# Kernel tuning notes

Measured on AMD Instinct MI355X. Metric: run time of the kernel, lower is better.

Reference implementation:

```python
import jax, jax.numpy as jnp
import numpy as np

NUM_HEADS = 16
D_MODEL = 1024
TEMPERATURE = D_MODEL ** 0.5  # note: module uses d_model**0.5, not head_dim**0.5


def setup_inputs() -> dict:
    key = jax.random.key(0)
    ks = jax.random.split(key, 8)
    B, T, D = 2, 2048, D_MODEL
    q = jax.random.normal(ks[0], (B, T, D), dtype=jnp.float32)
    k = jax.random.normal(ks[1], (B, T, D), dtype=jnp.float32)
    v = jax.random.normal(ks[2], (B, T, D), dtype=jnp.float32)
    # causal mask (tril) as suggested by the module docstring
    mask = jnp.tril(jnp.ones((T, T), dtype=bool))
    s = 1.0 / np.sqrt(D)
    Wq = jax.random.normal(ks[3], (D, D), dtype=jnp.float32) * s
    Wk = jax.random.normal(ks[4], (D, D), dtype=jnp.float32) * s
    Wv = jax.random.normal(ks[5], (D, D), dtype=jnp.float32) * s
    Wc = jax.random.normal(ks[6], (D, D), dtype=jnp.float32) * s
    return {"q": q, "k": k, "v": v, "Wq": Wq, "Wk": Wk, "Wv": Wv, "Wc": Wc, "mask": mask}


def reference(q, k, v, Wq, Wk, Wv, Wc, mask):
    B, T, D = q.shape
    H = NUM_HEADS
    hd = D // H
    # torch Linear (no bias): y = x @ W.T ; then split heads -> [B,H,T,hd]
    def proj(x, W):
        return (x @ W.T).reshape(B, T, H, hd).transpose(0, 2, 1, 3)
    qh, kh, vh = proj(q, Wq), proj(k, Wk), proj(v, Wv)
    # scores [B,H,T,T]
    scores = jnp.einsum("bhqd,bhkd->bhqk", qh / TEMPERATURE, kh)
    scores = jnp.where(mask, scores, -jnp.inf)
    attention = jax.nn.softmax(scores, axis=-1)  # dropout = identity (eval)
    out = jnp.einsum("bhqk,bhkd->bhqd", attention, vh)
    out = out.transpose(0, 2, 1, 3).reshape(B, T, D)
    out = out @ Wc.T  # combine projection; dropout = identity (eval)
    return (out, attention)
```

## Files before the change

kernel.cpp:

```cpp
#include <hip/hip_runtime.h>
#include <stdint.h>

typedef unsigned short u16;
typedef __bf16 bf16x8 __attribute__((ext_vector_type(8)));
typedef float f32x4 __attribute__((ext_vector_type(4)));

#define MFMA16(a, b, c) __builtin_amdgcn_mfma_f32_16x16x32_bf16((a), (b), (c), 0, 0, 0)

__device__ __forceinline__ u16 f2bf(float f) {
  union { __bf16 h; u16 u; } v;
  v.h = (__bf16)f;
  return v.u;
}

__device__ __forceinline__ float expf_c(float x) {
  return __expf(fmaxf(x, -80.0f));
}

struct Cvt6Args {
  const float* s0; const float* s1; const float* s2;
  const float* s3; const float* s4; const float* s5;
  u16* d0; u16* d1; u16* d2; u16* d3; u16* d4; u16* d5;
};

__global__ __launch_bounds__(256) void cvt6(Cvt6Args a) {
  const int z = blockIdx.y;
  const float* s; u16* d; int n8;
  if (z == 0)      { s = a.s0; d = a.d0; n8 = (4 * 1024 * 1024) / 8; }
  else if (z == 1) { s = a.s1; d = a.d1; n8 = (4 * 1024 * 1024) / 8; }
  else if (z == 2) { s = a.s2; d = a.d2; n8 = (4 * 1024 * 1024) / 8; }
  else if (z == 3) { s = a.s3; d = a.d3; n8 = (1024 * 1024) / 8; }
  else if (z == 4) { s = a.s4; d = a.d4; n8 = (1024 * 1024) / 8; }
  else             { s = a.s5; d = a.d5; n8 = (1024 * 1024) / 8; }
  const int i = blockIdx.x * 256 + threadIdx.x;
  if (i >= n8) return;
  float4 f0 = ((const float4*)s)[2 * i];
  float4 f1 = ((const float4*)s)[2 * i + 1];
  ushort4 h0, h1;
  h0.x = f2bf(f0.x); h0.y = f2bf(f0.y); h0.z = f2bf(f0.z); h0.w = f2bf(f0.w);
  h1.x = f2bf(f1.x); h1.y = f2bf(f1.y); h1.z = f2bf(f1.z); h1.w = f2bf(f1.w);
  ((ushort4*)d)[2 * i] = h0;
  ((ushort4*)d)[2 * i + 1] = h1;
}

__global__ __launch_bounds__(256) void cvt_one(const float* __restrict__ s,
                                               u16* __restrict__ d) {
  const int i = blockIdx.x * 256 + threadIdx.x;
  if (i >= (1024 * 1024) / 8) return;
  float4 f0 = ((const float4*)s)[2 * i];
  float4 f1 = ((const float4*)s)[2 * i + 1];
  ushort4 h0, h1;
  h0.x = f2bf(f0.x); h0.y = f2bf(f0.y); h0.z = f2bf(f0.z); h0.w = f2bf(f0.w);
  h1.x = f2bf(f1.x); h1.y = f2bf(f1.y); h1.z = f2bf(f1.z); h1.w = f2bf(f1.w);
  ((ushort4*)d)[2 * i] = h0;
  ((ushort4*)d)[2 * i + 1] = h1;
}

__device__ __forceinline__ void gemm_core(const u16* __restrict__ X,
                                          const u16* __restrict__ W,
                                          void* __restrict__ Yv, float scale,
                                          int omode) {
  __shared__ __align__(16) u16 lA[128 * 40];
  __shared__ __align__(16) u16 lB[128 * 40];
  const int tid = threadIdx.x;
  const int lane = tid & 63, w = tid >> 6;
  const int l15 = lane & 15, quad = lane >> 4;
  const int wm = (w >> 1) * 64, wn = (w & 1) * 64;
  const int m0 = blockIdx.x * 128, n0 = blockIdx.y * 128;

  f32x4 acc[4][4];
#pragma unroll
  for (int m = 0; m < 4; ++m)
#pragma unroll
    for (int n = 0; n < 4; ++n) acc[m][n] = (f32x4){0.f, 0.f, 0.f, 0.f};

  const int brow = tid >> 2, bseg = (tid & 3) * 8;

  for (int kk = 0; kk < 1024; kk += 32) {
    __syncthreads();
#pragma unroll
    for (int p = 0; p < 2; ++p) {
      int row = p * 64 + brow;
      *(uint4*)&lA[row * 40 + bseg] =
          *(const uint4*)&X[(size_t)(m0 + row) * 1024 + kk + bseg];
      *(uint4*)&lB[row * 40 + bseg] =
          *(const uint4*)&W[(size_t)(n0 + row) * 1024 + kk + bseg];
    }
    __syncthreads();
    bf16x8 af[4], bfr[4];
#pragma unroll
    for (int m = 0; m < 4; ++m)
      af[m] = *(const bf16x8*)&lA[(wm + m * 16 + l15) * 40 + quad * 8];
#pragma unroll
    for (int n = 0; n < 4; ++n)
      bfr[n] = *(const bf16x8*)&lB[(wn + n * 16 + l15) * 40 + quad * 8];
#pragma unroll
    for (int m = 0; m < 4; ++m)
#pragma unroll
      for (int n = 0; n < 4; ++n) acc[m][n] = MFMA16(af[m], bfr[n], acc[m][n]);
  }

  if (omode == 0) {
    u16* Y = (u16*)Yv;
#pragma unroll
    for (int m = 0; m < 4; ++m) {
      int grow0 = m0 + wm + m * 16 + quad * 4;
#pragma unroll
      for (int n = 0; n < 4; ++n) {
        int gcol = n0 + wn + n * 16 + l15;
#pragma unroll
        for (int r = 0; r < 4; ++r)
          Y[(size_t)(grow0 + r) * 1024 + gcol] = f2bf(acc[m][n][r] * scale);
      }
    }
  } else if (omode == 1) {
    u16* Y = (u16*)Yv;
#pragma unroll
    for (int m = 0; m < 4; ++m) {
      int grow0 = m0 + wm + m * 16 + quad * 4;
      int bb = grow0 >> 11, t = grow0 & 2047;
#pragma unroll
      for (int n = 0; n < 4; ++n) {
        int gcol = n0 + wn + n * 16 + l15;
        int hh = gcol >> 6, e = gcol & 63;
        ushort4 pk;
        pk.x = f2bf(acc[m][n][0]);
        pk.y = f2bf(acc[m][n][1]);
        pk.z = f2bf(acc[m][n][2]);
        pk.w = f2bf(acc[m][n][3]);
        *(ushort4*)&Y[((size_t)((bb * 16 + hh) * 64 + e)) * 2048 + t] = pk;
      }
    }
  } else {
    float* Y = (float*)Yv;
#pragma unroll
    for (int m = 0; m < 4; ++m) {
      int grow0 = m0 + wm + m * 16 + quad * 4;
#pragma unroll
      for (int n = 0; n < 4; ++n) {
        int gcol = n0 + wn + n * 16 + l15;
#pragma unroll
        for (int r = 0; r < 4; ++r)
          Y[(size_t)(grow0 + r) * 1024 + gcol] = acc[m][n][r] * scale;
      }
    }
  }
}

struct QKVArgs {
  const u16* X0; const u16* X1; const u16* X2;
  const u16* W0; const u16* W1; const u16* W2;
  void* Y0; void* Y1; void* Y2;
  float s0, s1, s2;
};

__global__ __launch_bounds__(256, 2) void proj_qkv(QKVArgs a) {
  const u16* X; const u16* W; void* Y; float sc; int om;
  if (blockIdx.z == 0)      { X = a.X0; W = a.W0; Y = a.Y0; sc = a.s0; om = 0; }
  else if (blockIdx.z == 1) { X = a.X1; W = a.W1; Y = a.Y1; sc = a.s1; om = 0; }
  else                      { X = a.X2; W = a.W2; Y = a.Y2; sc = a.s2; om = 1; }
  gemm_core(X, W, Y, sc, om);
}

__global__ __launch_bounds__(256, 2) void proj_out(const u16* __restrict__ Xv,
                                                   const u16* __restrict__ W,
                                                   void* __restrict__ Yv) {
  gemm_core(Xv, W, Yv, 1.0f, 2);
}

__global__ __launch_bounds__(256, 4) void attn_kernel(const u16* __restrict__ Qb,
                                                      const u16* __restrict__ Kb,
                                                      const u16* __restrict__ Vt,
                                                      float* __restrict__ attnF,
                                                      u16* __restrict__ Ob) {
  __shared__ __align__(16) u16 lK[64 * 72];
  __shared__ __align__(16) u16 lV[64 * 72];
  __shared__ __align__(16) u16 lP[4][16 * 72];

  const int bid = blockIdx.x;
  const int qt = bid >> 5;
  const int bh = bid & 31;
  const int b = bh >> 4, h = bh & 15;
  const int q0 = qt * 64;
  const int tid = threadIdx.x;
  const int w = tid >> 6, lane = tid & 63;
  const int l15 = lane & 15, quad = lane >> 4;
  const f32x4 ZERO4 = {0.f, 0.f, 0.f, 0.f};

  {
    const int kz0 = q0 + 64;
    if (kz0 < 2048) {
      for (int r = w; r < 64; r += 4) {
        size_t base = ((size_t)bh * 2048 + q0 + r) * 2048;
        uint4 z = {0, 0, 0, 0};
        for (int c = kz0 + lane * 4; c < 2048; c += 256)
          *(uint4*)&attnF[base + c] = z;
      }
    }
  }

  const int qrow = q0 + w * 16 + l15;
  const size_t qrowbase = (size_t)(b * 2048 + qrow) * 1024 + h * 64;
  const bf16x8 aq0 = *(const bf16x8*)&Qb[qrowbase + quad * 8];
  const bf16x8 aq1 = *(const bf16x8*)&Qb[qrowbase + 32 + quad * 8];

  const int kq = quad * 4;
  const int srow = tid >> 3, sseg = (tid & 7) * 8;

  float lacc = 0.f;
  for (int c = 0; c <= qt; ++c) {
    const int k0 = c * 64;
    __syncthreads();
#pragma unroll
    for (int p = 0; p < 2; ++p) {
      int rr = p * 32 + srow;
      *(uint4*)&lK[rr * 72 + sseg] =
          *(const uint4*)&Kb[(size_t)(b * 2048 + k0 + rr) * 1024 + h * 64 + sseg];
    }
    __syncthreads();
#pragma unroll
    for (int n = 0; n < 4; ++n) {
      bf16x8 bk0 = *(const bf16x8*)&lK[(n * 16 + l15) * 72 + quad * 8];
      bf16x8 bk1 = *(const bf16x8*)&lK[(n * 16 + l15) * 72 + 32 + quad * 8];
      f32x4 s = MFMA16(bk0, aq0, ZERO4);
      s = MFMA16(bk1, aq1, s);
      const int keyb = k0 + n * 16 + kq;
      if (c == qt) {
#pragma unroll
        for (int i = 0; i < 4; ++i)
          lacc += (keyb + i > qrow) ? 0.f : expf_c(s[i]);
      } else {
#pragma unroll
        for (int i = 0; i < 4; ++i) lacc += expf_c(s[i]);
      }
    }
  }
  lacc += __shfl_xor(lacc, 16);
  lacc += __shfl_xor(lacc, 32);
  const float invl = 1.0f / fmaxf(lacc, 1e-30f);

  f32x4 o[4];
#pragma unroll
  for (int n = 0; n < 4; ++n) o[n] = ZERO4;
  const size_t arow = ((size_t)bh * 2048 + qrow) * 2048;
  u16* lPw = lP[w];

  for (int c = 0; c <= qt; ++c) {
    const int k0 = c * 64;
    __syncthreads();
#pragma unroll
    for (int p = 0; p < 2; ++p) {
      int rr = p * 32 + srow;
      *(uint4*)&lK[rr * 72 + sseg] =
          *(const uint4*)&Kb[(size_t)(b * 2048 + k0 + rr) * 1024 + h * 64 + sseg];
      *(uint4*)&lV[rr * 72 + sseg] =
          *(const uint4*)&Vt[((size_t)bh * 64 + rr) * 2048 + k0 + sseg];
    }
    __syncthreads();
    const bool diag = (c == qt);
#pragma unroll
    for (int n = 0; n < 4; ++n) {
      bf16x8 bk0 = *(const bf16x8*)&lK[(n * 16 + l15) * 72 + quad * 8];
      bf16x8 bk1 = *(const bf16x8*)&lK[(n * 16 + l15) * 72 + 32 + quad * 8];
      f32x4 s = MFMA16(bk0, aq0, ZERO4);
      s = MFMA16(bk1, aq1, s);
      const int keyb = k0 + n * 16 + kq;
#pragma unroll
      for (int i = 0; i < 4; ++i) {
        float pv = expf_c(s[i]) * invl;
        if (diag && keyb + i > qrow) pv = 0.f;
        s[i] = pv;
      }
      *(f32x4*)&attnF[arow + keyb] = s;
      ushort4 pk;
      pk.x = f2bf(s[0]); pk.y = f2bf(s[1]); pk.z = f2bf(s[2]); pk.w = f2bf(s[3]);
      *(ushort4*)&lPw[l15 * 72 + n * 16 + kq] = pk;
    }
#pragma unroll
    for (int kkk = 0; kkk < 2; ++kkk) {
      bf16x8 ap = *(const bf16x8*)&lPw[l15 * 72 + kkk * 32 + quad * 8];
#pragma unroll
      for (int n = 0; n < 4; ++n) {
        bf16x8 bv = *(const bf16x8*)&lV[(n * 16 + l15) * 72 + kkk * 32 + quad * 8];
        o[n] = MFMA16(ap, bv, o[n]);
      }
    }
  }

#pragma unroll
  for (int n = 0; n < 4; ++n)
#pragma unroll
    for (int i = 0; i < 4; ++i) {
      float ov = o[n][i];
      if (!(ov == ov)) ov = 0.f;
      lPw[(quad * 4 + i) * 72 + n * 16 + l15] = f2bf(ov);
    }
  {
    int prow = lane >> 3, pseg = (lane & 7) * 8;
#pragma unroll
    for (int p2 = 0; p2 < 2; ++p2) {
      int rr = p2 * 8 + prow;
      *(uint4*)&Ob[(size_t)(b * 2048 + q0 + w * 16 + rr) * 1024 + h * 64 + pseg] =
          *(const uint4*)&lPw[rr * 72 + pseg];
    }
  }
}

extern "C" void kernel_launch(void* const* d_in, const int* in_sizes, int n_in,
                              void* d_out, int out_size, void* d_ws, size_t ws_size,
                              hipStream_t stream) {
  const float* q  = (const float*)d_in[0];
  const float* k  = (const float*)d_in[1];
  const float* v  = (const float*)d_in[2];
  const float* Wq = (const float*)d_in[3];
  const float* Wk = (const float*)d_in[4];
  const float* Wv = (const float*)d_in[5];
  const float* Wc = (const float*)d_in[6];

  float* outF  = (float*)d_out;
  float* attnF = outF + (size_t)4096 * 1024;

  const size_t BUF  = (size_t)4096 * 1024;
  const size_t WBUF = (size_t)1024 * 1024;
  u16* ws = (u16*)d_ws;
  const bool big_ws = ws_size >= 4 * BUF * sizeof(u16);

  u16 *Qb, *Kb, *Vt, *Ob;
  if (big_ws) {
    Qb = ws; Kb = ws + BUF; Vt = ws + 2 * BUF; Ob = ws + 3 * BUF;
  } else {
    Qb = (u16*)outF; Ob = (u16*)outF + BUF; Kb = ws; Vt = ws + BUF;
  }

  u16* qbf  = (u16*)attnF;
  u16* kbf  = qbf  + BUF;
  u16* vbf  = kbf  + BUF;
  u16* wqbf = vbf  + BUF;
  u16* wkbf = wqbf + WBUF;
  u16* wvbf = wkbf + WBUF;
  u16* wcbf = Vt;

  dim3 blk(256, 1, 1);

  Cvt6Args ca;
  ca.s0 = q;    ca.s1 = k;    ca.s2 = v;
  ca.s3 = Wq;   ca.s4 = Wk;   ca.s5 = Wv;
  ca.d0 = qbf;  ca.d1 = kbf;  ca.d2 = vbf;
  ca.d3 = wqbf; ca.d4 = wkbf; ca.d5 = wvbf;
  cvt6<<<dim3(2048, 6), blk, 0, stream>>>(ca);

  QKVArgs a;
  a.X0 = qbf;  a.X1 = kbf;  a.X2 = vbf;
  a.W0 = wqbf; a.W1 = wkbf; a.W2 = wvbf;
  a.Y0 = Qb; a.Y1 = Kb; a.Y2 = Vt;
  a.s0 = 0.03125f;
  a.s1 = 1.0f; a.s2 = 1.0f;
  proj_qkv<<<dim3(32, 8, 3), blk, 0, stream>>>(a);
  attn_kernel<<<dim3(1024), blk, 0, stream>>>(Qb, Kb, Vt, attnF, Ob);

  cvt_one<<<dim3(512), blk, 0, stream>>>(Wc, wcbf);

  const u16* gemm_src = Ob;
  if (!big_ws) {
    (void)hipMemcpyAsync(ws, Ob, BUF * sizeof(u16), hipMemcpyDeviceToDevice, stream);
    gemm_src = ws;
  }
  proj_out<<<dim3(32, 8), blk, 0, stream>>>(gemm_src, wcbf, outF);
}
```

Measured before the change: 744.2 us.

## Load GEMM tiles directly to LDS with XOR swizzle and K=64 steps

Replaces the register-staged global-to-LDS copy in the projection GEMM core with global_load_lds direct transfers, doubles the K step per iteration to 64, and uses an XOR-swizzled LDS layout instead of row padding to avoid bank conflicts. It aims to cut VGPR traffic and halve the number of barrier pairs per K loop. The kernel is still single-buffered with no overlap, and it depends on the direct-to-LDS lane layout matching the swizzle.

New measurement: 733.9 us. About the same (-1.4%).

```diff
diff --git a/kernel.cpp b/kernel.cpp
--- a/kernel.cpp
+++ b/kernel.cpp
@@ -15,6 +15,12 @@
 
 __device__ __forceinline__ float expf_c(float x) {
   return __expf(fmaxf(x, -80.0f));
+}
+
+__device__ __forceinline__ void gl_lds16(const u16* g, u16* l) {
+  __builtin_amdgcn_global_load_lds(
+      (const __attribute__((address_space(1))) unsigned int*)g,
+      (__attribute__((address_space(3))) unsigned int*)l, 16, 0, 0);
 }
 
 struct Cvt6Args {
@@ -60,8 +66,8 @@
                                           const u16* __restrict__ W,
                                           void* __restrict__ Yv, float scale,
                                           int omode) {
-  __shared__ __align__(16) u16 lA[128 * 40];
-  __shared__ __align__(16) u16 lB[128 * 40];
+  __shared__ __align__(16) u16 lA[128 * 64];
+  __shared__ __align__(16) u16 lB[128 * 64];
   const int tid = threadIdx.x;
   const int lane = tid & 63, w = tid >> 6;
   const int l15 = lane & 15, quad = lane >> 4;
@@ -74,30 +80,37 @@
 #pragma unroll
     for (int n = 0; n < 4; ++n) acc[m][n] = (f32x4){0.f, 0.f, 0.f, 0.f};
 
-  const int brow = tid >> 2, bseg = (tid & 3) * 8;
-
-  for (int kk = 0; kk < 1024; kk += 32) {
-    __syncthreads();
-#pragma unroll
-    for (int p = 0; p < 2; ++p) {
-      int row = p * 64 + brow;
-      *(uint4*)&lA[row * 40 + bseg] =
-          *(const uint4*)&X[(size_t)(m0 + row) * 1024 + kk + bseg];
-      *(uint4*)&lB[row * 40 + bseg] =
-          *(const uint4*)&W[(size_t)(n0 + row) * 1024 + kk + bseg];
-    }
-    __syncthreads();
-    bf16x8 af[4], bfr[4];
-#pragma unroll
-    for (int m = 0; m < 4; ++m)
-      af[m] = *(const bf16x8*)&lA[(wm + m * 16 + l15) * 40 + quad * 8];
-#pragma unroll
-    for (int n = 0; n < 4; ++n)
-      bfr[n] = *(const bf16x8*)&lB[(wn + n * 16 + l15) * 40 + quad * 8];
-#pragma unroll
-    for (int m = 0; m < 4; ++m)
-#pragma unroll
-      for (int n = 0; n < 4; ++n) acc[m][n] = MFMA16(af[m], bfr[n], acc[m][n]);
+  const int row8 = lane >> 3;
+  const int slot = lane & 7;
+  const int scol = ((slot ^ row8) << 3);
+
+  for (int kk = 0; kk < 1024; kk += 64) {
+    __syncthreads();
+#pragma unroll
+    for (int ps = 0; ps < 4; ++ps) {
+      const int seg = w * 4 + ps;
+      const int row = seg * 8 + row8;
+      gl_lds16(&X[(size_t)(m0 + row) * 1024 + kk + scol], &lA[seg * 512]);
+      gl_lds16(&W[(size_t)(n0 + row) * 1024 + kk + scol], &lB[seg * 512]);
+    }
+    __syncthreads();
+    bf16x8 af[2][4], bfr[2][4];
+#pragma unroll
+    for (int h = 0; h < 2; ++h)
+#pragma unroll
+      for (int m = 0; m < 4; ++m) {
+        const int rA = wm + m * 16 + l15;
+        const int rB = wn + m * 16 + l15;
+        af[h][m] = *(const bf16x8*)&lA[rA * 64 + (((quad + 4 * h) ^ (rA & 7)) << 3)];
+        bfr[h][m] = *(const bf16x8*)&lB[rB * 64 + (((quad + 4 * h) ^ (rB & 7)) << 3)];
+      }
+#pragma unroll
+    for (int h = 0; h < 2; ++h)
+#pragma unroll
+      for (int m = 0; m < 4; ++m)
+#pragma unroll
+        for (int n = 0; n < 4; ++n)
+          acc[m][n] = MFMA16(af[h][m], bfr[h][n], acc[m][n]);
   }
 
   if (omode == 0) {
```
